# Kernel tuning notes

Hardware: AMD Instinct MI355X
Metric: run time of the kernel (lower is better)

## Reference

```python
import jax, jax.numpy as jnp
import numpy as np

D_MODEL = 1024
NUM_HEADS = 16
ROPE_THETA = 10000.0


def _rope(v, pos, theta=ROPE_THETA):
    # v: [B, S, D] (full d_model, as in the original module), pos: [B, S] int
    d = v.shape[-1]
    inv_freq = theta ** (-jnp.arange(0, d, 2, dtype=jnp.float32) / d)  # [D/2]
    ang = pos.astype(jnp.float32)[..., None] * inv_freq  # [B, S, D/2]
    cos, sin = jnp.cos(ang), jnp.sin(ang)
    x1, x2 = v[..., ::2], v[..., 1::2]
    r1 = x1 * cos - x2 * sin
    r2 = x1 * sin + x2 * cos
    return jnp.stack([r1, r2], axis=-1).reshape(v.shape)


def setup_inputs() -> dict:
    key = jax.random.key(0)
    ks = jax.random.split(key, 6)
    B, S, D = 2, 2048, D_MODEL
    std = np.sqrt(2.0 / (D + D)).astype(np.float32)
    x = jax.random.normal(ks[0], (B, S, D), dtype=jnp.float32)
    token_positions = jnp.sort(jax.random.randint(ks[1], (B, S), 0, S), axis=-1).astype(jnp.int32)
    wq = jax.random.normal(ks[2], (D, D), dtype=jnp.float32) * std
    wk = jax.random.normal(ks[3], (D, D), dtype=jnp.float32) * std
    wv = jax.random.normal(ks[4], (D, D), dtype=jnp.float32) * std
    wo = jax.random.normal(ks[5], (D, D), dtype=jnp.float32) * std
    return {"x": x, "token_positions": token_positions, "wq": wq, "wk": wk, "wv": wv, "wo": wo}


def reference(x, token_positions, wq, wk, wv, wo):
    B, S, D = x.shape
    H = NUM_HEADS
    dk = D // H
    # Projections (nn.functional.linear: x @ W^T)
    q = x @ wq.T
    k = x @ wk.T
    v = x @ wv.T
    # In the original, Q/K are reshaped to heads and back before RoPE -> identity;
    # RoPE is applied over the FULL d_model dimension.
    q = _rope(q, token_positions)
    k = _rope(k, token_positions)
    # Split heads
    q = q.reshape(B, S, H, dk)
    k = k.reshape(B, S, H, dk)
    v = v.reshape(B, S, H, dk)
    scores = jnp.einsum('bqhd,bkhd->bhqk', q, k) / jnp.sqrt(jnp.asarray(dk, x.dtype))
    causal = jnp.tril(jnp.ones((S, S), dtype=bool))  # True where allowed
    scores = jnp.where(causal[None, None], scores, -jnp.inf)
    attn = jax.nn.softmax(scores, axis=-1)
    out = jnp.einsum('bhqk,bkhd->bqhd', attn, v).reshape(B, S, D)
    return out @ wo.T
```

## Files before the change

kernel.cpp:

```cpp
#include <hip/hip_runtime.h>
#include <hip/hip_bf16.h>
#include <math.h>

typedef __attribute__((ext_vector_type(8))) short bf16x8;
typedef __attribute__((ext_vector_type(4))) float f32x4;
typedef __attribute__((ext_vector_type(8))) float f32x8;

#define D_MODEL 1024
#define NHEADS  16
#define DK      64
#define BATCH   2
#define SEQ     2048

static __device__ __forceinline__ short f2bf(float f) {
    unsigned u = __builtin_bit_cast(unsigned, f);
    u = u + 0x7FFFu + ((u >> 16) & 1u);
    return (short)(u >> 16);
}
static __device__ __forceinline__ short f2bf_fast(float f) {
    return (short)((__builtin_bit_cast(unsigned, f) + 0x8000u) >> 16);
}
static __device__ __forceinline__ float bf2f(short s) {
    return __builtin_bit_cast(float, ((unsigned)(unsigned short)s) << 16);
}

typedef __attribute__((address_space(3))) unsigned int lds_uint;
typedef __attribute__((address_space(1))) const unsigned int glob_uint;
static __device__ __forceinline__ void gl2lds16(const short* g, short* l) {
    __builtin_amdgcn_global_load_lds((glob_uint*)g, (lds_uint*)l, 16, 0, 0);
}

__global__ void detect_kernel(const unsigned* __restrict__ x, int* __restrict__ flag)
{
    const int lane = threadIdx.x;
    const unsigned w = x[lane];
    const unsigned e = (w >> 7) & 0xFFu;
    const bool weird = (e >= 0x88u) || (e <= 0x5Fu);
    const unsigned long long m = __ballot(weird);
    if (lane == 0) *flag = (__popcll(m) >= 16) ? 1 : 0;
}

#define NX8 ((BATCH * SEQ * D_MODEL) / 8)
#define NW8 ((D_MODEL * D_MODEL) / 8)
__global__ void cvt_all_kernel(const void* __restrict__ x,  const void* __restrict__ wq,
                               const void* __restrict__ wk, const void* __restrict__ wv,
                               const void* __restrict__ wo,
                               __hip_bfloat16* __restrict__ xb,  __hip_bfloat16* __restrict__ wqb,
                               __hip_bfloat16* __restrict__ wkb, __hip_bfloat16* __restrict__ wvb,
                               __hip_bfloat16* __restrict__ wob,
                               const int* __restrict__ dtf)
{
    const int i = blockIdx.x * blockDim.x + threadIdx.x;
    if (i >= NX8 + 4 * NW8) return;
    const void* src; __hip_bfloat16* dst; int off;
    if (i < NX8) { src = x; dst = xb; off = i; }
    else {
        const int j = i - NX8, seg = j >> 17; off = j & (NW8 - 1);
        switch (seg) {
            case 0: src = wq; dst = wqb; break;
            case 1: src = wk; dst = wkb; break;
            case 2: src = wv; dst = wvb; break;
            default: src = wo; dst = wob; break;
        }
    }
    if (*dtf) {
        const f32x8 v = ((const f32x8*)src)[off];
        bf16x8 r;
#pragma unroll
        for (int j = 0; j < 8; ++j) r[j] = f2bf(v[j]);
        ((bf16x8*)dst)[off] = r;
    } else {
        ((bf16x8*)dst)[off] = ((const bf16x8*)src)[off];
    }
}

static __device__ __forceinline__ void gemm128_main(
    const short* __restrict__ A, const short* __restrict__ B,
    int K, int bm, int bn, f32x4 (&acc)[4][4], short* lds)
{
    const int tid  = threadIdx.x;
    const int lane = tid & 63;
    const int wave = tid >> 6;
    const int l16  = lane & 15;
    const int quad = lane >> 4;

    const int srow = lane >> 2;
    const int scg  = (lane & 3) ^ ((lane >> 3) & 3);
    const short* ag = A + (size_t)(bm + wave * 32 + srow) * K + scg * 8;
    const short* bg = B + (size_t)(bn + wave * 32 + srow) * K + scg * 8;
    const int dst = wave * 1024 + lane * 8;

    const int mrow = (wave >> 1) * 64;
    const int nrow = (wave & 1) * 64;
    const int ph   = ((quad ^ ((l16 >> 1) & 3))) * 8;

    auto stage = [&](int k0, int buf) {
        short* ad = lds + buf * 4096 + dst;
        short* bd = lds + 8192 + buf * 4096 + dst;
        gl2lds16(ag + k0, ad);
        gl2lds16(ag + k0 + (size_t)16 * K, ad + 512);
        gl2lds16(bg + k0, bd);
        gl2lds16(bg + k0 + (size_t)16 * K, bd + 512);
    };

    stage(0, 0);
    for (int k0 = 0, t = 0; k0 < K; k0 += 32, ++t) {
        __asm__ volatile("s_waitcnt vmcnt(0)" ::: "memory");
        __syncthreads();
        if (k0 + 32 < K) stage(k0 + 32, (t + 1) & 1);

        const short* Ab = lds + (t & 1) * 4096;
        const short* Bb = lds + 8192 + (t & 1) * 4096;
        bf16x8 a[4], b[4];
#pragma unroll
        for (int x = 0; x < 4; ++x)
            a[x] = *(const bf16x8*)(Ab + (mrow + x * 16 + l16) * 32 + ph);
#pragma unroll
        for (int y = 0; y < 4; ++y)
            b[y] = *(const bf16x8*)(Bb + (nrow + y * 16 + l16) * 32 + ph);
#pragma unroll
        for (int x = 0; x < 4; ++x)
#pragma unroll
            for (int y = 0; y < 4; ++y)
                acc[x][y] = __builtin_amdgcn_mfma_f32_16x16x32_bf16(
                    a[x], b[y], acc[x][y], 0, 0, 0);
    }
}

__global__ __launch_bounds__(256) void gemm_qkv_kernel(
    const __hip_bfloat16* __restrict__ xb,
    const __hip_bfloat16* __restrict__ wqb,
    const __hip_bfloat16* __restrict__ wkb,
    const __hip_bfloat16* __restrict__ wvb,
    __hip_bfloat16* __restrict__ Qb,
    __hip_bfloat16* __restrict__ Kb,
    __hip_bfloat16* __restrict__ Vt)
{
    __shared__ alignas(16) short lds[16384];
    const int wsel = blockIdx.x >> 3;
    const int bn   = (blockIdx.x & 7) * 128;
    const int bm   = blockIdx.y * 128;
    const short* W = (const short*)(wsel == 0 ? wqb : (wsel == 1 ? wkb : wvb));

    f32x4 acc[4][4];
#pragma unroll
    for (int x = 0; x < 4; ++x)
#pragma unroll
        for (int y = 0; y < 4; ++y) acc[x][y] = (f32x4){0.f, 0.f, 0.f, 0.f};

    gemm128_main((const short*)xb, W, D_MODEL, bm, bn, acc, lds);

    const int lane = threadIdx.x & 63;
    const int wave = threadIdx.x >> 6;
    const int l16  = lane & 15;
    const int quad = lane >> 4;
    __hip_bfloat16* Crm = (wsel == 1) ? Kb : Qb;

#pragma unroll
    for (int x = 0; x < 4; ++x)
#pragma unroll
        for (int y = 0; y < 4; ++y)
#pragma unroll
            for (int r = 0; r < 4; ++r) {
                const int row = bm + (wave >> 1) * 64 + x * 16 + quad * 4 + r;
                const int col = bn + (wave & 1) * 64 + y * 16 + l16;
                const __hip_bfloat16 v = __float2bfloat16(acc[x][y][r]);
                if (wsel == 2) {
                    const int hh = col >> 6, dcol = col & 63;
                    const int bb = row >> 11, ss = row & (SEQ - 1);
                    Vt[(((size_t)bb * NHEADS + hh) * DK + dcol) * SEQ + ss] = v;
                } else {
                    Crm[(size_t)row * D_MODEL + col] = v;
                }
            }
}

__global__ __launch_bounds__(256) void gemm_out_kernel(
    const __hip_bfloat16* __restrict__ AO,
    const __hip_bfloat16* __restrict__ wob,
    void* __restrict__ C, const int* __restrict__ dtf)
{
    __shared__ alignas(16) short lds[16384];
    const int bn = blockIdx.x * 128;
    const int bm = blockIdx.y * 128;
    const bool c32 = (*dtf) != 0;

    f32x4 acc[4][4];
#pragma unroll
    for (int x = 0; x < 4; ++x)
#pragma unroll
        for (int y = 0; y < 4; ++y) acc[x][y] = (f32x4){0.f, 0.f, 0.f, 0.f};

    gemm128_main((const short*)AO, (const short*)wob, D_MODEL, bm, bn, acc, lds);

    const int lane = threadIdx.x & 63;
    const int wave = threadIdx.x >> 6;
    const int l16  = lane & 15;
    const int quad = lane >> 4;

#pragma unroll
    for (int x = 0; x < 4; ++x)
#pragma unroll
        for (int y = 0; y < 4; ++y)
#pragma unroll
            for (int r = 0; r < 4; ++r) {
                const int row = bm + (wave >> 1) * 64 + x * 16 + quad * 4 + r;
                const int col = bn + (wave & 1) * 64 + y * 16 + l16;
                const size_t idx = (size_t)row * D_MODEL + col;
                if (c32) ((float*)C)[idx] = acc[x][y][r];
                else     ((__hip_bfloat16*)C)[idx] = __float2bfloat16(acc[x][y][r]);
            }
}

__global__ void rope_kernel(__hip_bfloat16* __restrict__ Q,
                            __hip_bfloat16* __restrict__ Kt,
                            const int* __restrict__ pos, int n8)
{
    const int idx = blockIdx.x * blockDim.x + threadIdx.x;
    if (idx >= n8) return;
    const int elem0 = idx * 8;
    const int bs = elem0 >> 10;
    const int i0 = (elem0 & (D_MODEL - 1)) >> 1;

    const float p = (float)pos[bs];
    bf16x8 q8 = *((bf16x8*)Q + idx);
    bf16x8 k8 = *((bf16x8*)Kt + idx);

#pragma unroll
    for (int j = 0; j < 4; ++j) {
        const float inv = exp2f((float)(i0 + j) * -0.02595256257f);
        const float ang = p * inv;
        const float c = cosf(ang), s = sinf(ang);
        const float q1 = bf2f(q8[2 * j]);
        const float q2 = bf2f(q8[2 * j + 1]);
        const float k1 = bf2f(k8[2 * j]);
        const float k2 = bf2f(k8[2 * j + 1]);
        q8[2 * j]     = f2bf(q1 * c - q2 * s);
        q8[2 * j + 1] = f2bf(q1 * s + q2 * c);
        k8[2 * j]     = f2bf(k1 * c - k2 * s);
        k8[2 * j + 1] = f2bf(k1 * s + k2 * c);
    }
    *((bf16x8*)Q + idx)  = q8;
    *((bf16x8*)Kt + idx) = k8;
}

__global__ __launch_bounds__(256) void flash_attn_kernel(
    __hip_bfloat16* QO,
    const __hip_bfloat16* __restrict__ Kt,
    const __hip_bfloat16* __restrict__ Vt)
{
    __shared__ alignas(16) short k_lds[2][64 * 64];
    __shared__ alignas(16) short v_lds[2][64 * 64];
    __shared__ alignas(16) short p_lds[4][16 * 72];

    const int lane = threadIdx.x & 63;
    const int wave = threadIdx.x >> 6;
    const int l16  = lane & 15;
    const int quad = lane >> 4;
    const int qtA  = blockIdx.x;
    const int qtB  = 31 - qtA;
    const int b    = blockIdx.y / NHEADS;
    const int h    = blockIdx.y % NHEADS;
    const size_t base  = (size_t)b * SEQ * D_MODEL + h * DK;
    const size_t vbase = (size_t)blockIdx.y * DK * SEQ;

    const short* Qp = (const short*)QO;
    const short* Kp = (const short*)Kt;
    const short* Vp = (const short*)Vt;

    const int qA0 = qtA * 64 + wave * 16;
    const int qB0 = qtB * 64 + wave * 16;
    const bf16x8 aqA0 = *(const bf16x8*)(Qp + base + (size_t)(qA0 + l16) * D_MODEL + quad * 8);
    const bf16x8 aqA1 = *(const bf16x8*)(Qp + base + (size_t)(qA0 + l16) * D_MODEL + 32 + quad * 8);
    const bf16x8 aqB0 = *(const bf16x8*)(Qp + base + (size_t)(qB0 + l16) * D_MODEL + quad * 8);
    const bf16x8 aqB1 = *(const bf16x8*)(Qp + base + (size_t)(qB0 + l16) * D_MODEL + 32 + quad * 8);

    f32x4 oA[4], oB[4];
    float lA[4] = {0.f, 0.f, 0.f, 0.f}, lB[4] = {0.f, 0.f, 0.f, 0.f};
#pragma unroll
    for (int g = 0; g < 4; ++g) { oA[g] = (f32x4){0.f,0.f,0.f,0.f}; oB[g] = (f32x4){0.f,0.f,0.f,0.f}; }

    const int srow = lane >> 3;
    const int scg  = (lane & 7) ^ srow;
    const int dst  = wave * 512 + lane * 8;
    const short* kg = Kp + ((size_t)b * SEQ + wave * 8 + srow) * D_MODEL + h * DK + scg * 8;
    const short* vg = Vp + vbase + (size_t)(wave * 8 + srow) * SEQ + scg * 8;

    const int ph0 = (quad ^ (l16 & 7)) * 8;
    const int ph1 = ((4 + quad) ^ (l16 & 7)) * 8;

    auto stage = [&](int t, int buf) {
        const int kv0 = t * 64;
        gl2lds16(kg + (size_t)kv0 * D_MODEL, k_lds[buf] + dst);
        gl2lds16(kg + (size_t)(kv0 + 32) * D_MODEL, k_lds[buf] + 2048 + dst);
        gl2lds16(vg + kv0, v_lds[buf] + dst);
        gl2lds16(vg + kv0 + (size_t)32 * SEQ, v_lds[buf] + 2048 + dst);
    };

    auto process = [&](int buf, int kv0, int q0, bool masked,
                       const bf16x8& aq0, const bf16x8& aq1,
                       f32x4 (&o)[4], float (&ls)[4]) {
        const short* kb = k_lds[buf];
        const short* vb = v_lds[buf];
        f32x4 sfrag[4];
#pragma unroll
        for (int g = 0; g < 4; ++g) {
            const int rowk = (g * 16 + l16) * 64;
            const bf16x8 bk0 = *(const bf16x8*)(kb + rowk + ph0);
            const bf16x8 bk1 = *(const bf16x8*)(kb + rowk + ph1);
            f32x4 c = (f32x4){0.f, 0.f, 0.f, 0.f};
            c = __builtin_amdgcn_mfma_f32_16x16x32_bf16(aq0, bk0, c, 0, 0, 0);
            c = __builtin_amdgcn_mfma_f32_16x16x32_bf16(aq1, bk1, c, 0, 0, 0);
            sfrag[g] = c;
        }
#pragma unroll
        for (int r = 0; r < 4; ++r) {
            const int qrow = q0 + quad * 4 + r;
            float ps = 0.f;
#pragma unroll
            for (int g = 0; g < 4; ++g) {
                float p = __expf(sfrag[g][r] * 0.125f);
                if (masked && (kv0 + g * 16 + l16 > qrow)) p = 0.f;
                ps += p;
                p_lds[wave][(quad * 4 + r) * 72 + g * 16 + l16] = f2bf_fast(p);
            }
            ls[r] += ps;
        }
        __asm__ volatile("s_waitcnt lgkmcnt(0)" ::: "memory");
        const bf16x8 ap0 = *(const bf16x8*)(&p_lds[wave][l16 * 72 + quad * 8]);
        const bf16x8 ap1 = *(const bf16x8*)(&p_lds[wave][l16 * 72 + 32 + quad * 8]);
#pragma unroll
        for (int g = 0; g < 4; ++g) {
            const int rowv = (g * 16 + l16) * 64;
            const bf16x8 bv0 = *(const bf16x8*)(vb + rowv + ph0);
            const bf16x8 bv1 = *(const bf16x8*)(vb + rowv + ph1);
            o[g] = __builtin_amdgcn_mfma_f32_16x16x32_bf16(ap0, bv0, o[g], 0, 0, 0);
            o[g] = __builtin_amdgcn_mfma_f32_16x16x32_bf16(ap1, bv1, o[g], 0, 0, 0);
        }
    };

    const int tiles = qtB + 1;
    stage(0, 0);
    for (int t = 0; t < tiles; ++t) {
        __asm__ volatile("s_waitcnt vmcnt(0)" ::: "memory");
        __syncthreads();
        if (t + 1 < tiles) stage(t + 1, (t + 1) & 1);

        const int kv0 = t * 64;
        const int buf = t & 1;
        if (t <= qtA) process(buf, kv0, qA0, t == qtA, aqA0, aqA1, oA, lA);
        process(buf, kv0, qB0, t == qtB, aqB0, aqB1, oB, lB);
    }

#pragma unroll
    for (int r = 0; r < 4; ++r) {
        float sa = lA[r], sb = lB[r];
#pragma unroll
        for (int off = 1; off < 16; off <<= 1) {
            sa += __shfl_xor(sa, off);
            sb += __shfl_xor(sb, off);
        }
        lA[r] = sa; lB[r] = sb;
    }
#pragma unroll
    for (int g = 0; g < 4; ++g)
#pragma unroll
        for (int r = 0; r < 4; ++r) {
            const int rowA = qA0 + quad * 4 + r;
            const int rowB = qB0 + quad * 4 + r;
            QO[base + (size_t)rowA * D_MODEL + g * 16 + l16] =
                __float2bfloat16(oA[g][r] / fmaxf(lA[r], 1e-20f));
            QO[base + (size_t)rowB * D_MODEL + g * 16 + l16] =
                __float2bfloat16(oB[g][r] / fmaxf(lB[r], 1e-20f));
        }
}

extern "C" void kernel_launch(void* const* d_in, const int* in_sizes, int n_in,
                              void* d_out, int out_size, void* d_ws, size_t ws_size,
                              hipStream_t stream)
{
    (void)in_sizes; (void)n_in; (void)out_size; (void)ws_size;

    const void* x  = d_in[0];
    const int*  pos = (const int*)d_in[1];
    const void* wq = d_in[2];
    const void* wk = d_in[3];
    const void* wv = d_in[4];
    const void* wo = d_in[5];

    const int M = BATCH * SEQ;
    const int D = D_MODEL;
    const size_t MD = (size_t)M * D;
    const size_t DD = (size_t)D * D;

    int* dtf = (int*)d_ws;
    __hip_bfloat16* xb  = (__hip_bfloat16*)((char*)d_ws + 256);
    __hip_bfloat16* wqb = xb  + MD;
    __hip_bfloat16* wkb = wqb + DD;
    __hip_bfloat16* wvb = wkb + DD;
    __hip_bfloat16* wob = wvb + DD;
    __hip_bfloat16* Qb  = wob + DD;
    __hip_bfloat16* Vtb = Qb  + MD;
    __hip_bfloat16* Kb  = (__hip_bfloat16*)d_out;

    dim3 blk(256);

    hipLaunchKernelGGL(detect_kernel, dim3(1), dim3(64), 0, stream,
                       (const unsigned*)x, dtf);

    const int ncvt = NX8 + 4 * NW8;
    hipLaunchKernelGGL(cvt_all_kernel, dim3((ncvt + 255) / 256), blk, 0, stream,
                       x, wq, wk, wv, wo, xb, wqb, wkb, wvb, wob, dtf);

    hipLaunchKernelGGL(gemm_qkv_kernel, dim3(24, 32), blk, 0, stream,
                       xb, wqb, wkb, wvb, Qb, Kb, Vtb);

    const int nrope8 = (int)(MD / 8);
    hipLaunchKernelGGL(rope_kernel, dim3((nrope8 + 255) / 256), blk, 0, stream,
                       Qb, Kb, pos, nrope8);

    hipLaunchKernelGGL(flash_attn_kernel, dim3(SEQ / 128, BATCH * NHEADS), blk, 0, stream,
                       Qb, Kb, Vtb);

    hipLaunchKernelGGL(gemm_out_kernel, dim3(D / 128, M / 128), blk, 0, stream,
                       Qb, wob, d_out, dtf);
}
```

Baseline: 202.4 us.

## Shrink GEMM tiles to 64x128 and inline dtype detection into kernels

Both projection GEMMs now use 64x128 block tiles, with each wave owning a 64x32 slice, instead of 128x128 tiles. This doubles the block count (768 to 1536 for QKV, 256 to 512 for the output GEMM) so the GPU's compute units are better filled. The separate dtype-detection kernel is removed and each convert/output block recomputes the fp32 check with a wave ballot, saving a launch and a dependent flag read. In exchange, each output element gets less operand reuse from LDS, and every block does a redundant 64-element global read for detection.

```diff
diff --git a/kernel.cpp b/kernel.cpp
--- a/kernel.cpp
+++ b/kernel.cpp
@@ -30,14 +30,12 @@
     __builtin_amdgcn_global_load_lds((glob_uint*)g, (lds_uint*)l, 16, 0, 0);
 }
 
-__global__ void detect_kernel(const unsigned* __restrict__ x, int* __restrict__ flag)
-{
-    const int lane = threadIdx.x;
-    const unsigned w = x[lane];
+static __device__ __forceinline__ bool detect_fp32(const unsigned* __restrict__ x)
+{
+    const unsigned w = x[threadIdx.x & 63];
     const unsigned e = (w >> 7) & 0xFFu;
     const bool weird = (e >= 0x88u) || (e <= 0x5Fu);
-    const unsigned long long m = __ballot(weird);
-    if (lane == 0) *flag = (__popcll(m) >= 16) ? 1 : 0;
+    return __popcll(__ballot(weird)) >= 16;
 }
 
 #define NX8 ((BATCH * SEQ * D_MODEL) / 8)
@@ -47,9 +45,9 @@
                                const void* __restrict__ wo,
                                __hip_bfloat16* __restrict__ xb,  __hip_bfloat16* __restrict__ wqb,
                                __hip_bfloat16* __restrict__ wkb, __hip_bfloat16* __restrict__ wvb,
-                               __hip_bfloat16* __restrict__ wob,
-                               const int* __restrict__ dtf)
-{
+                               __hip_bfloat16* __restrict__ wob)
+{
+    const bool f32 = detect_fp32((const unsigned*)x);
     const int i = blockIdx.x * blockDim.x + threadIdx.x;
     if (i >= NX8 + 4 * NW8) return;
     const void* src; __hip_bfloat16* dst; int off;
@@ -63,7 +61,7 @@
             default: src = wo; dst = wob; break;
         }
     }
-    if (*dtf) {
+    if (f32) {
         const f32x8 v = ((const f32x8*)src)[off];
         bf16x8 r;
 #pragma unroll
@@ -74,9 +72,9 @@
     }
 }
 
-static __device__ __forceinline__ void gemm128_main(
+static __device__ __forceinline__ void gemm64x128_main(
     const short* __restrict__ A, const short* __restrict__ B,
-    int K, int bm, int bn, f32x4 (&acc)[4][4], short* lds)
+    int K, int bm, int bn, f32x4 (&acc)[4][2], short (&lds)[2][6144])
 {
     const int tid  = threadIdx.x;
     const int lane = tid & 63;
@@ -86,21 +84,16 @@
 
     const int srow = lane >> 2;
     const int scg  = (lane & 3) ^ ((lane >> 3) & 3);
-    const short* ag = A + (size_t)(bm + wave * 32 + srow) * K + scg * 8;
+    const short* ag = A + (size_t)(bm + wave * 16 + srow) * K + scg * 8;
     const short* bg = B + (size_t)(bn + wave * 32 + srow) * K + scg * 8;
-    const int dst = wave * 1024 + lane * 8;
-
-    const int mrow = (wave >> 1) * 64;
-    const int nrow = (wave & 1) * 64;
+
+    const int nrow = wave * 32;
     const int ph   = ((quad ^ ((l16 >> 1) & 3))) * 8;
 
     auto stage = [&](int k0, int buf) {
-        short* ad = lds + buf * 4096 + dst;
-        short* bd = lds + 8192 + buf * 4096 + dst;
-        gl2lds16(ag + k0, ad);
-        gl2lds16(ag + k0 + (size_t)16 * K, ad + 512);
-        gl2lds16(bg + k0, bd);
-        gl2lds16(bg + k0 + (size_t)16 * K, bd + 512);
+        gl2lds16(ag + k0, &lds[buf][wave * 512 + lane * 8]);
+        gl2lds16(bg + k0, &lds[buf][2048 + wave * 1024 + lane * 8]);
+        gl2lds16(bg + k0 + (size_t)16 * K, &lds[buf][2048 + wave * 1024 + 512 + lane * 8]);
     };
 
     stage(0, 0);
@@ -109,21 +102,21 @@
         __syncthreads();
         if (k0 + 32 < K) stage(k0 + 32, (t + 1) & 1);
 
-        const short* Ab = lds + (t & 1) * 4096;
-        const short* Bb = lds + 8192 + (t & 1) * 4096;
-        bf16x8 a[4], b[4];
-#pragma unroll
-        for (int x = 0; x < 4; ++x)
-            a[x] = *(const bf16x8*)(Ab + (mrow + x * 16 + l16) * 32 + ph);
-#pragma unroll
-        for (int y = 0; y < 4; ++y)
+        const short* Ab = &lds[t & 1][0];
+        const short* Bb = &lds[t & 1][2048];
+        bf16x8 a[4], b[2];
+#pragma unroll
+        for (int xx = 0; xx < 4; ++xx)
+            a[xx] = *(const bf16x8*)(Ab + (xx * 16 + l16) * 32 + ph);
+#pragma unroll
+        for (int y = 0; y < 2; ++y)
             b[y] = *(const bf16x8*)(Bb + (nrow + y * 16 + l16) * 32 + ph);
 #pragma unroll
-        for (int x = 0; x < 4; ++x)
-#pragma unroll
-            for (int y = 0; y < 4; ++y)
-                acc[x][y] = __builtin_amdgcn_mfma_f32_16x16x32_bf16(
-                    a[x], b[y], acc[x][y], 0, 0, 0);
+        for (int xx = 0; xx < 4; ++xx)
+#pragma unroll
+            for (int y = 0; y < 2; ++y)
+                acc[xx][y] = __builtin_amdgcn_mfma_f32_16x16x32_bf16(
+                    a[xx], b[y], acc[xx][y], 0, 0, 0);
     }
 }
 
@@ -136,19 +129,19 @@
     __hip_bfloat16* __restrict__ Kb,
     __hip_bfloat16* __restrict__ Vt)
 {
-    __shared__ alignas(16) short lds[16384];
+    __shared__ alignas(16) short lds[2][6144];
     const int wsel = blockIdx.x >> 3;
     const int bn   = (blockIdx.x & 7) * 128;
-    const int bm   = blockIdx.y * 128;
+    const int bm   = blockIdx.y * 64;
     const short* W = (const short*)(wsel == 0 ? wqb : (wsel == 1 ? wkb : wvb));
 
-    f32x4 acc[4][4];
-#pragma unroll
-    for (int x = 0; x < 4; ++x)
-#pragma unroll
-        for (int y = 0; y < 4; ++y) acc[x][y] = (f32x4){0.f, 0.f, 0.f, 0.f};
-
-    gemm128_main((const short*)xb, W, D_MODEL, bm, bn, acc, lds);
+    f32x4 acc[4][2];
+#pragma unroll
+    for (int xx = 0; xx < 4; ++xx)
+#pragma unroll
+        for (int y = 0; y < 2; ++y) acc[xx][y] = (f32x4){0.f, 0.f, 0.f, 0.f};
+
+    gemm64x128_main((const short*)xb, W, D_MODEL, bm, bn, acc, lds);
 
     const int lane = threadIdx.x & 63;
     const int wave = threadIdx.x >> 6;
@@ -157,14 +150,14 @@
     __hip_bfloat16* Crm = (wsel == 1) ? Kb : Qb;
 
 #pragma unroll
-    for (int x = 0; x < 4; ++x)
-#pragma unroll
-        for (int y = 0; y < 4; ++y)
+    for (int xx = 0; xx < 4; ++xx)
+#pragma unroll
+        for (int y = 0; y < 2; ++y)
 #pragma unroll
             for (int r = 0; r < 4; ++r) {
-                const int row = bm + (wave >> 1) * 64 + x * 16 + quad * 4 + r;
-                const int col = bn + (wave & 1) * 64 + y * 16 + l16;
-                const __hip_bfloat16 v = __float2bfloat16(acc[x][y][r]);
+                const int row = bm + xx * 16 + quad * 4 + r;
+                const int col = bn + wave * 32 + y * 16 + l16;
+                const __hip_bfloat16 v = __float2bfloat16(acc[xx][y][r]);
                 if (wsel == 2) {
                     const int hh = col >> 6, dcol = col & 63;
                     const int bb = row >> 11, ss = row & (SEQ - 1);
@@ -178,20 +171,20 @@
 __global__ __launch_bounds__(256) void gemm_out_kernel(
     const __hip_bfloat16* __restrict__ AO,
     const __hip_bfloat16* __restrict__ wob,
-    void* __restrict__ C, const int* __restrict__ dtf)
-{
-    __shared__ alignas(16) short lds[16384];
+    void* __restrict__ C, const unsigned* __restrict__ xdet)
+{
+    __shared__ alignas(16) short lds[2][6144];
+    const bool c32 = detect_fp32(xdet);
     const int bn = blockIdx.x * 128;
-    const int bm = blockIdx.y * 128;
-    const bool c32 = (*dtf) != 0;
-
-    f32x4 acc[4][4];
-#pragma unroll
-    for (int x = 0; x < 4; ++x)
-#pragma unroll
-        for (int y = 0; y < 4; ++y) acc[x][y] = (f32x4){0.f, 0.f, 0.f, 0.f};
-
-    gemm128_main((const short*)AO, (const short*)wob, D_MODEL, bm, bn, acc, lds);
+    const int bm = blockIdx.y * 64;
+
+    f32x4 acc[4][2];
+#pragma unroll
+    for (int xx = 0; xx < 4; ++xx)
+#pragma unroll
+        for (int y = 0; y < 2; ++y) acc[xx][y] = (f32x4){0.f, 0.f, 0.f, 0.f};
+
+    gemm64x128_main((const short*)AO, (const short*)wob, D_MODEL, bm, bn, acc, lds);
 
     const int lane = threadIdx.x & 63;
     const int wave = threadIdx.x >> 6;
@@ -199,16 +192,16 @@
     const int quad = lane >> 4;
 
 #pragma unroll
-    for (int x = 0; x < 4; ++x)
-#pragma unroll
-        for (int y = 0; y < 4; ++y)
+    for (int xx = 0; xx < 4; ++xx)
+#pragma unroll
+        for (int y = 0; y < 2; ++y)
 #pragma unroll
             for (int r = 0; r < 4; ++r) {
-                const int row = bm + (wave >> 1) * 64 + x * 16 + quad * 4 + r;
-                const int col = bn + (wave & 1) * 64 + y * 16 + l16;
+                const int row = bm + xx * 16 + quad * 4 + r;
+                const int col = bn + wave * 32 + y * 16 + l16;
                 const size_t idx = (size_t)row * D_MODEL + col;
-                if (c32) ((float*)C)[idx] = acc[x][y][r];
-                else     ((__hip_bfloat16*)C)[idx] = __float2bfloat16(acc[x][y][r]);
+                if (c32) ((float*)C)[idx] = acc[xx][y][r];
+                else     ((__hip_bfloat16*)C)[idx] = __float2bfloat16(acc[xx][y][r]);
             }
 }
 
@@ -393,8 +386,7 @@
     const size_t MD = (size_t)M * D;
     const size_t DD = (size_t)D * D;
 
-    int* dtf = (int*)d_ws;
-    __hip_bfloat16* xb  = (__hip_bfloat16*)((char*)d_ws + 256);
+    __hip_bfloat16* xb  = (__hip_bfloat16*)d_ws;
     __hip_bfloat16* wqb = xb  + MD;
     __hip_bfloat16* wkb = wqb + DD;
     __hip_bfloat16* wvb = wkb + DD;
@@ -405,14 +397,11 @@
 
     dim3 blk(256);
 
-    hipLaunchKernelGGL(detect_kernel, dim3(1), dim3(64), 0, stream,
-                       (const unsigned*)x, dtf);
-
     const int ncvt = NX8 + 4 * NW8;
     hipLaunchKernelGGL(cvt_all_kernel, dim3((ncvt + 255) / 256), blk, 0, stream,
-                       x, wq, wk, wv, wo, xb, wqb, wkb, wvb, wob, dtf);
-
-    hipLaunchKernelGGL(gemm_qkv_kernel, dim3(24, 32), blk, 0, stream,
+                       x, wq, wk, wv, wo, xb, wqb, wkb, wvb, wob);
+
+    hipLaunchKernelGGL(gemm_qkv_kernel, dim3(24, 64), blk, 0, stream,
                        xb, wqb, wkb, wvb, Qb, Kb, Vtb);
 
     const int nrope8 = (int)(MD / 8);
@@ -422,6 +411,6 @@
     hipLaunchKernelGGL(flash_attn_kernel, dim3(SEQ / 128, BATCH * NHEADS), blk, 0, stream,
                        Qb, Kb, Vtb);
 
-    hipLaunchKernelGGL(gemm_out_kernel, dim3(D / 128, M / 128), blk, 0, stream,
-                       Qb, wob, d_out, dtf);
-}
+    hipLaunchKernelGGL(gemm_out_kernel, dim3(D / 128, M / 64), blk, 0, stream,
+                       Qb, wob, d_out, (const unsigned*)x);
+}
```

Result: slower. 211.8 us (+4.7%).
